# Performance work log

Hardware: AMD Instinct MI355X
Metric: run time of the kernel (lower is better)

Reference implementation:

```python
import jax, jax.numpy as jnp
import numpy as np

N_NODES = 100000


def gcn_conv(x, W, b, src, dst, n_nodes):
    """PyG-style GCNConv: add self-loops, symmetric normalization, aggregate to dst."""
    x = x @ W  # [N, out]
    loop = jnp.arange(n_nodes, dtype=src.dtype)
    src_sl = jnp.concatenate([src, loop])  # [E+N]
    dst_sl = jnp.concatenate([dst, loop])
    deg = jax.ops.segment_sum(jnp.ones(src_sl.shape[0], x.dtype), dst_sl,
                              num_segments=n_nodes)  # [N]
    dinv = jnp.where(deg > 0, jax.lax.rsqrt(deg), 0.0)
    norm = dinv[src_sl] * dinv[dst_sl]  # [E+N]
    msg = x[src_sl] * norm[:, None]  # gather + scale
    out = jax.ops.segment_sum(msg, dst_sl, num_segments=n_nodes)  # scatter-add
    return out + b


def setup_inputs() -> dict:
    key = jax.random.key(0)
    ks = jax.random.split(key, 8)
    in_d, hid_d, out_d = 64, 128, 64
    x = jax.random.normal(ks[0], (N_NODES, in_d), dtype=jnp.float32)
    edge_index = jax.random.randint(ks[1], (2, 1000000), 0, N_NODES, dtype=jnp.int64)
    s1 = 1.0 / np.sqrt(in_d)
    s2 = 1.0 / np.sqrt(hid_d)
    sc = 1.0 / np.sqrt(2 * out_d)
    W1 = jax.random.uniform(ks[2], (in_d, hid_d), jnp.float32, -s1, s1)
    b1 = jnp.zeros((hid_d,), jnp.float32)
    W2 = jax.random.uniform(ks[3], (hid_d, out_d), jnp.float32, -s2, s2)
    b2 = jnp.zeros((out_d,), jnp.float32)
    Wc = jax.random.uniform(ks[4], (2 * out_d, 1), jnp.float32, -sc, sc)
    bc = jax.random.uniform(ks[5], (1,), jnp.float32, -sc, sc)
    return {"x": x, "edge_index": edge_index, "W1": W1, "b1": b1,
            "W2": W2, "b2": b2, "Wc": Wc, "bc": bc}


def reference(x, edge_index, W1, b1, W2, b2, Wc, bc):
    src, dst = edge_index[0], edge_index[1]
    h = jax.nn.relu(gcn_conv(x, W1, b1, src, dst, N_NODES))
    h = jax.nn.relu(gcn_conv(h, W2, b2, src, dst, N_NODES))
    # edge-level gather-concat-linear-sigmoid
    edge_emb = jnp.concatenate([h[src], h[dst]], axis=1)  # [E, 2*out_d]
    logits = edge_emb @ Wc + bc  # [E, 1]
    return jax.nn.sigmoid(logits)
```

## Files before the change

### kernel.cpp

```cpp
#include <hip/hip_runtime.h>
#include <hip/hip_fp16.h>
#include <math.h>

#define IN_D 64
#define HID_D 128
#define OUT_D 64

typedef _Float16 half8 __attribute__((ext_vector_type(8)));
typedef float f32x4 __attribute__((ext_vector_type(4)));

#define ECAP   16384
#define CSRCAP (ECAP + 512 * 3)
#define DCHUNK 2048

__global__ void k_init(int* __restrict__ bcur,
                       const float* __restrict__ W1, const float* __restrict__ W2,
                       __half* __restrict__ w1f, __half* __restrict__ w2f,
                       __half* __restrict__ xs, __half* __restrict__ ts,
                       int N, int nbuk) {
    int t = blockIdx.x * 256 + threadIdx.x;
    if (blockIdx.x == 0 && threadIdx.x < nbuk)
        bcur[threadIdx.x] = threadIdx.x * ECAP;
    if (t < 2048) {
        int which = t >> 10, fl = t & 1023;
        int f = fl >> 6, l = fl & 63, q = l >> 4, n16 = l & 15;
        if (which == 0) {
            int nt = f >> 1, kc = f & 1, n = nt * 16 + n16, k0 = kc * 32 + q * 8;
            for (int j = 0; j < 8; ++j)
                w1f[(size_t)fl * 8 + j] = __float2half(W1[(k0 + j) * 128 + n]);
        } else {
            int nt = f >> 2, kc = f & 3, n = nt * 16 + n16, k0 = kc * 32 + q * 8;
            for (int j = 0; j < 8; ++j)
                w2f[(size_t)fl * 8 + j] = __float2half(W2[(k0 + j) * 64 + n]);
        }
    } else {
        int si = t - 2048;
        if (si < 64) {
            xs[(size_t)N * 64 + si] = __float2half(0.f);
            ts[(size_t)N * 64 + si] = __float2half(0.f);
        }
    }
}

__global__ __launch_bounds__(256) void k_decode3(const unsigned int* __restrict__ raw,
                                                 int E,
                                                 int* __restrict__ bcur,
                                                 int2* __restrict__ pairs) {
    __shared__ int hist[256];
    __shared__ int base[256];
    __shared__ int cnt[256];
    __shared__ int is64s;
    if (threadIdx.x == 0) {
        int f = 1;
        for (int i = 1; i < 64; i += 2) f &= (raw[i] == 0u);
        is64s = f;
    }
    hist[threadIdx.x] = 0; cnt[threadIdx.x] = 0;
    __syncthreads();
    int is64 = is64s;
    int e0 = blockIdx.x * DCHUNK;
    int s[8], d[8], b[8];
    if ((E & 1) == 0) {
#pragma unroll
        for (int i = 0; i < 4; ++i) {
            int e = e0 + (threadIdx.x + i * 256) * 2;
            if (e < E) {
                int s0, d0, s1, d1;
                if (is64) {
                    uint4 sv = *(const uint4*)&raw[2 * (size_t)e];
                    uint4 dv = *(const uint4*)&raw[2 * ((size_t)E + e)];
                    s0 = (int)sv.x; s1 = (int)sv.z;
                    d0 = (int)dv.x; d1 = (int)dv.z;
                } else {
                    uint2 sv = *(const uint2*)&raw[e];
                    uint2 dv = *(const uint2*)&raw[E + e];
                    s0 = (int)sv.x; s1 = (int)sv.y;
                    d0 = (int)dv.x; d1 = (int)dv.y;
                }
                s[2 * i] = s0; d[2 * i] = d0; b[2 * i] = d0 >> 9;
                s[2 * i + 1] = s1; d[2 * i + 1] = d1; b[2 * i + 1] = d1 >> 9;
                atomicAdd(&hist[b[2 * i]], 1);
                atomicAdd(&hist[b[2 * i + 1]], 1);
            } else { b[2 * i] = -1; b[2 * i + 1] = -1; }
        }
    } else {
#pragma unroll
        for (int i = 0; i < 8; ++i) {
            int e = e0 + threadIdx.x + i * 256;
            if (e < E) {
                int sv, dv;
                if (is64) {
                    sv = (int)raw[2 * (size_t)e];
                    dv = (int)raw[2 * ((size_t)E + e)];
                } else {
                    sv = (int)raw[e];
                    dv = (int)raw[E + e];
                }
                s[i] = sv; d[i] = dv; b[i] = dv >> 9;
                atomicAdd(&hist[b[i]], 1);
            } else b[i] = -1;
        }
    }
    __syncthreads();
    if (hist[threadIdx.x] > 0)
        base[threadIdx.x] = atomicAdd(&bcur[threadIdx.x], hist[threadIdx.x]);
    __syncthreads();
#pragma unroll
    for (int i = 0; i < 8; ++i) {
        if (b[i] >= 0) {
            int pos = base[b[i]] + atomicAdd(&cnt[b[i]], 1);
            pairs[pos] = make_int2(s[i], d[i]);
        }
    }
}

__global__ __launch_bounds__(256) void k_build(const int2* __restrict__ pairs,
                                               const int* __restrict__ bcur,
                                               int2* __restrict__ prowdeg,
                                               int* __restrict__ csr_src,
                                               float* __restrict__ dinv,
                                               const float* __restrict__ x,
                                               __half* __restrict__ xs,
                                               int N) {
    __shared__ int deg5[512];
    __shared__ int cur5[512];
    __shared__ int wsum[4];
    int b = blockIdx.x;
    int n0 = b << 9;
    int n1 = n0 + 512; if (n1 > N) n1 = N;
    int nn = n1 - n0;
    deg5[threadIdx.x] = 0;
    deg5[threadIdx.x + 256] = 0;
    __syncthreads();
    int beg = b * ECAP, end = bcur[b];
    for (int i = beg + threadIdx.x; i < end; i += 256)
        atomicAdd(&deg5[pairs[i].y - n0], 1);
    __syncthreads();
    int pbase = b * CSRCAP;
    int t = threadIdx.x;
    int v0 = deg5[2 * t], v1 = deg5[2 * t + 1];
    int p0 = (v0 + 3) & ~3, p1 = (v1 + 3) & ~3;
    int s = p0 + p1;
    int lane = t & 63, w = t >> 6;
    int inc = s;
    for (int off = 1; off < 64; off <<= 1) {
        int n = __shfl_up(inc, off);
        if (lane >= off) inc += n;
    }
    if (lane == 63) wsum[w] = inc;
    __syncthreads();
    for (int k = 0; k < w; ++k) inc += wsum[k];
    int ex0 = inc - s, ex1 = inc - p1;
    int ps0 = pbase + ex0, ps1 = pbase + ex1;
    cur5[2 * t] = ps0;
    cur5[2 * t + 1] = ps1;
    if (2 * t < nn) {
        prowdeg[n0 + 2 * t] = make_int2(ps0, p0);
        dinv[n0 + 2 * t] = rsqrtf((float)v0 + 1.0f);
    }
    if (2 * t + 1 < nn) {
        prowdeg[n0 + 2 * t + 1] = make_int2(ps1, p1);
        dinv[n0 + 2 * t + 1] = rsqrtf((float)v1 + 1.0f);
    }
    __syncthreads();
    for (int i = beg + threadIdx.x; i < end; i += 256) {
        int2 r = pairs[i];
        int pos = atomicAdd(&cur5[r.y - n0], 1);
        csr_src[pos] = r.x;
    }
    __syncthreads();
    for (int i = cur5[2 * t]; i < ps0 + p0; ++i) csr_src[i] = N;
    for (int i = cur5[2 * t + 1]; i < ps1 + p1; ++i) csr_src[i] = N;
    for (int idx = t; idx < nn * 8; idx += 256) {
        int i = idx >> 3, c8 = (idx & 7) * 8;
        int node = n0 + i;
        float di = rsqrtf((float)deg5[i] + 1.0f);
        float4 va = *(const float4*)&x[(size_t)node * 64 + c8];
        float4 vb = *(const float4*)&x[(size_t)node * 64 + c8 + 4];
        union { __half2 h[4]; uint4 u; } pk2;
        pk2.h[0] = __floats2half2_rn(va.x * di, va.y * di);
        pk2.h[1] = __floats2half2_rn(va.z * di, va.w * di);
        pk2.h[2] = __floats2half2_rn(vb.x * di, vb.y * di);
        pk2.h[3] = __floats2half2_rn(vb.z * di, vb.w * di);
        *(uint4*)&xs[(size_t)node * 64 + c8] = pk2.u;
    }
}

__global__ __launch_bounds__(256) void k_gather1(const __half* __restrict__ xs,
                          const float* __restrict__ dinv,
                          const int2* __restrict__ prowdeg, const int* __restrict__ csr,
                          __half* __restrict__ agg, int N) {
    int wv = threadIdx.x >> 6, l = threadIdx.x & 63;
    int ns = l >> 3, seg = l & 7;
    int node = (blockIdx.x * 4 + wv) * 8 + ns;
    bool valid = node < N;
    int nc = valid ? node : N - 1;
    int2 rp = prowdeg[nc];
    int beg = rp.x;
    int pend = beg + (valid ? rp.y : 0);
    float di = dinv[nc];
    half8 hs = *(const half8*)&xs[(size_t)nc * 64 + seg * 8];
    float acc[8];
#pragma unroll
    for (int j = 0; j < 8; ++j) acc[j] = 0.f;
    for (int k = beg; k < pend; k += 4) {
        int4 s4 = *(const int4*)&csr[k];
        half8 h0 = *(const half8*)&xs[(size_t)s4.x * 64 + seg * 8];
        half8 h1 = *(const half8*)&xs[(size_t)s4.y * 64 + seg * 8];
        half8 h2 = *(const half8*)&xs[(size_t)s4.z * 64 + seg * 8];
        half8 h3 = *(const half8*)&xs[(size_t)s4.w * 64 + seg * 8];
#pragma unroll
        for (int j = 0; j < 8; ++j) {
            float t01 = (float)h0[j] + (float)h1[j];
            float t23 = (float)h2[j] + (float)h3[j];
            acc[j] += t01 + t23;
        }
    }
    if (valid) {
        half8 o;
#pragma unroll
        for (int j = 0; j < 8; ++j) o[j] = (_Float16)((acc[j] + (float)hs[j]) * di);
        *(half8*)&agg[(size_t)node * 64 + seg * 8] = o;
    }
}

__global__ __launch_bounds__(256) void k_gather2(const __half* __restrict__ ts,
                          const float* __restrict__ dinv,
                          const int2* __restrict__ prowdeg, const int* __restrict__ csr,
                          const float* __restrict__ b2, const float* __restrict__ Wc,
                          float* __restrict__ s0o, float* __restrict__ s1o, int N) {
    int wv = threadIdx.x >> 6, l = threadIdx.x & 63;
    int ns = l >> 3, seg = l & 7;
    int node = (blockIdx.x * 4 + wv) * 8 + ns;
    bool valid = node < N;
    int nc = valid ? node : N - 1;
    int2 rp = prowdeg[nc];
    int beg = rp.x;
    int pend = beg + (valid ? rp.y : 0);
    float di = dinv[nc];
    half8 hs = *(const half8*)&ts[(size_t)nc * 64 + seg * 8];
    float acc[8];
#pragma unroll
    for (int j = 0; j < 8; ++j) acc[j] = 0.f;
    for (int k = beg; k < pend; k += 4) {
        int4 s4 = *(const int4*)&csr[k];
        half8 h0 = *(const half8*)&ts[(size_t)s4.x * 64 + seg * 8];
        half8 h1 = *(const half8*)&ts[(size_t)s4.y * 64 + seg * 8];
        half8 h2 = *(const half8*)&ts[(size_t)s4.z * 64 + seg * 8];
        half8 h3 = *(const half8*)&ts[(size_t)s4.w * 64 + seg * 8];
#pragma unroll
        for (int j = 0; j < 8; ++j) {
            float t01 = (float)h0[j] + (float)h1[j];
            float t23 = (float)h2[j] + (float)h3[j];
            acc[j] += t01 + t23;
        }
    }
    {
        float4 b2a = *(const float4*)&b2[seg * 8];
        float4 b2b = *(const float4*)&b2[seg * 8 + 4];
        float4 w0a = *(const float4*)&Wc[seg * 8];
        float4 w0b = *(const float4*)&Wc[seg * 8 + 4];
        float4 w1a = *(const float4*)&Wc[64 + seg * 8];
        float4 w1b = *(const float4*)&Wc[64 + seg * 8 + 4];
        float bb[8] = {b2a.x, b2a.y, b2a.z, b2a.w, b2b.x, b2b.y, b2b.z, b2b.w};
        float w0[8] = {w0a.x, w0a.y, w0a.z, w0a.w, w0b.x, w0b.y, w0b.z, w0b.w};
        float w1[8] = {w1a.x, w1a.y, w1a.z, w1a.w, w1b.x, w1b.y, w1b.z, w1b.w};
        float p0 = 0.f, p1 = 0.f;
#pragma unroll
        for (int j = 0; j < 8; ++j) {
            float v = fmaxf((acc[j] + (float)hs[j]) * di + bb[j], 0.f);
            p0 = fmaf(v, w0[j], p0);
            p1 = fmaf(v, w1[j], p1);
        }
        p0 += __shfl_xor(p0, 1); p1 += __shfl_xor(p1, 1);
        p0 += __shfl_xor(p0, 2); p1 += __shfl_xor(p1, 2);
        p0 += __shfl_xor(p0, 4); p1 += __shfl_xor(p1, 4);
        if (seg == 0 && valid) { s0o[node] = p0; s1o[node] = p1; }
    }
}

__global__ __launch_bounds__(256) void k_mlp_mfma(const __half* __restrict__ agg_h,
                                                  const __half* __restrict__ w1f,
                                                  const __half* __restrict__ w2f,
                                                  const float* __restrict__ b1,
                                                  const float* __restrict__ dinv,
                                                  __half* __restrict__ ts, int N) {
    __shared__ __align__(16) __half w1l[8192];
    __shared__ __align__(16) __half w2l[8192];
    {
        const float4* sA = (const float4*)w1f;
        const float4* sB = (const float4*)w2f;
        float4* dA = (float4*)w1l;
        float4* dB = (float4*)w2l;
        for (int i = threadIdx.x; i < 1024; i += 256) { dA[i] = sA[i]; dB[i] = sB[i]; }
    }
    __syncthreads();

    int wv = threadIdx.x >> 6, l = threadIdx.x & 63;
    int m0 = blockIdx.x * 64 + wv * 16;
    if (m0 >= N) return;
    int q = l >> 4, ml = l & 15;
    int rowA = m0 + ml; if (rowA >= N) rowA = N - 1;

    half8 bfr0 = *(const half8*)&agg_h[(size_t)rowA * 64 + q * 8];
    half8 bfr1 = *(const half8*)&agg_h[(size_t)rowA * 64 + 32 + q * 8];

    int pk[8][2];
#pragma unroll
    for (int nt = 0; nt < 8; ++nt) {
        float4 bb = *(const float4*)&b1[nt * 16 + q * 4];
        f32x4 cacc; cacc[0] = bb.x; cacc[1] = bb.y; cacc[2] = bb.z; cacc[3] = bb.w;
        half8 a0 = *(const half8*)&w1l[(nt * 2 + 0) * 512 + l * 8];
        cacc = __builtin_amdgcn_mfma_f32_16x16x32_f16(a0, bfr0, cacc, 0, 0, 0);
        half8 a1 = *(const half8*)&w1l[(nt * 2 + 1) * 512 + l * 8];
        cacc = __builtin_amdgcn_mfma_f32_16x16x32_f16(a1, bfr1, cacc, 0, 0, 0);
        union { __half2 h; int i; } u0, u1;
        u0.h = __floats2half2_rn(fmaxf(cacc[0], 0.f), fmaxf(cacc[1], 0.f));
        u1.h = __floats2half2_rn(fmaxf(cacc[2], 0.f), fmaxf(cacc[3], 0.f));
        pk[nt][0] = u0.i;
        pk[nt][1] = u1.i;
    }

    int src0 = ml + 16 * ((2 * q) & 3);
    int src1 = ml + 16 * ((2 * q + 1) & 3);
    bool hi = (q >= 2);
    half8 afr[4];
#pragma unroll
    for (int kc = 0; kc < 4; ++kc) {
        int t0 = 2 * kc, t1 = 2 * kc + 1;
        int d0a = __shfl(pk[t0][0], src0), d0b = __shfl(pk[t1][0], src0);
        int d1a = __shfl(pk[t0][1], src0), d1b = __shfl(pk[t1][1], src0);
        int d2a = __shfl(pk[t0][0], src1), d2b = __shfl(pk[t1][0], src1);
        int d3a = __shfl(pk[t0][1], src1), d3b = __shfl(pk[t1][1], src1);
        union { int d[4]; half8 h; } u;
        u.d[0] = hi ? d0b : d0a;
        u.d[1] = hi ? d1b : d1a;
        u.d[2] = hi ? d2b : d2a;
        u.d[3] = hi ? d3b : d3a;
        afr[kc] = u.h;
    }

    float dl = dinv[rowA];
    float dv[4];
#pragma unroll
    for (int r = 0; r < 4; ++r) dv[r] = __shfl(dl, q * 4 + r);

#pragma unroll
    for (int nt2 = 0; nt2 < 4; ++nt2) {
        f32x4 cacc; cacc[0] = 0.f; cacc[1] = 0.f; cacc[2] = 0.f; cacc[3] = 0.f;
#pragma unroll
        for (int kc = 0; kc < 4; ++kc) {
            half8 b = *(const half8*)&w2l[(nt2 * 4 + kc) * 512 + l * 8];
            cacc = __builtin_amdgcn_mfma_f32_16x16x32_f16(afr[kc], b, cacc, 0, 0, 0);
        }
#pragma unroll
        for (int r = 0; r < 4; ++r) {
            int node = m0 + q * 4 + r;
            if (node < N)
                ts[(size_t)node * 64 + nt2 * 16 + ml] = __float2half(cacc[r] * dv[r]);
        }
    }
}

__global__ void k_edge(const unsigned int* __restrict__ raw,
                       const float* __restrict__ s0, const float* __restrict__ s1,
                       const float* __restrict__ bc, float* __restrict__ out, int E) {
    __shared__ int is64s;
    if (threadIdx.x == 0) {
        int f = 1;
        for (int i = 1; i < 64; i += 2) f &= (raw[i] == 0u);
        is64s = f;
    }
    __syncthreads();
    int is64 = is64s;
    int e = (blockIdx.x * blockDim.x + threadIdx.x) * 2;
    if (e >= E) return;
    float b = bc[0];
    if (((E & 1) == 0) && (e + 1 < E)) {
        int sa, sb, da, db;
        if (is64) {
            uint4 sv = *(const uint4*)&raw[2 * (size_t)e];
            uint4 dv = *(const uint4*)&raw[2 * ((size_t)E + e)];
            sa = (int)sv.x; sb = (int)sv.z;
            da = (int)dv.x; db = (int)dv.z;
        } else {
            uint2 sv = *(const uint2*)&raw[e];
            uint2 dv = *(const uint2*)&raw[E + e];
            sa = (int)sv.x; sb = (int)sv.y;
            da = (int)dv.x; db = (int)dv.y;
        }
        float z0 = s0[sa] + s1[da] + b;
        float z1 = s0[sb] + s1[db] + b;
        float2 o;
        o.x = 1.0f / (1.0f + __expf(-z0));
        o.y = 1.0f / (1.0f + __expf(-z1));
        *(float2*)&out[e] = o;
    } else {
        for (int k = e; k < E && k < e + 2; ++k) {
            int sa, da;
            if (is64) {
                sa = (int)raw[2 * (size_t)k];
                da = (int)raw[2 * ((size_t)E + k)];
            } else {
                sa = (int)raw[k];
                da = (int)raw[E + k];
            }
            float z = s0[sa] + s1[da] + b;
            out[k] = 1.0f / (1.0f + __expf(-z));
        }
    }
}

extern "C" void kernel_launch(void* const* d_in, const int* in_sizes, int n_in,
                              void* d_out, int out_size, void* d_ws, size_t ws_size,
                              hipStream_t stream) {
    const float* x  = (const float*)d_in[0];
    const unsigned int* eidx = (const unsigned int*)d_in[1];
    const float* W1 = (const float*)d_in[2];
    const float* b1 = (const float*)d_in[3];
    const float* W2 = (const float*)d_in[4];
    const float* b2 = (const float*)d_in[5];
    const float* Wc = (const float*)d_in[6];
    const float* bc = (const float*)d_in[7];
    float* out = (float*)d_out;

    int N = in_sizes[0] / IN_D;
    int E = in_sizes[1] / 2;
    int nbuk = (N + 511) >> 9;
    int nchunk = (E + DCHUNK - 1) / DCHUNK;

    char* p = (char*)d_ws;
    int*   bcur    = (int*)p;    p += 256 * 4;
    int*   csr_src = (int*)p;    p += (size_t)nbuk * CSRCAP * 4;
    float* dinv    = (float*)p;  p += (size_t)N * 4;
    float* s0      = (float*)p;  p += (size_t)N * 4;
    float* s1      = (float*)p;  p += (size_t)N * 4;
    p += 15; p = (char*)((size_t)p & ~(size_t)15);
    int2*  prowdeg = (int2*)p;   p += (size_t)N * 8;
    int2*  pairs   = (int2*)p;   p += (size_t)nbuk * ECAP * 8;
    __half* xs    = (__half*)p;  p += (size_t)(N + 1) * 64 * 2;
    __half* aggh  = (__half*)p;  p += (size_t)N * 64 * 2;
    __half* ts    = (__half*)p;  p += (size_t)(N + 1) * 64 * 2;
    __half* w1f   = (__half*)p;  p += 8192 * 2;
    __half* w2f   = (__half*)p;  p += 8192 * 2;

    k_init<<<9, 256, 0, stream>>>(bcur, W1, W2, w1f, w2f, xs, ts, N, nbuk);
    k_decode3<<<nchunk, 256, 0, stream>>>(eidx, E, bcur, pairs);
    k_build<<<nbuk, 256, 0, stream>>>(pairs, bcur, prowdeg, csr_src, dinv, x, xs, N);

    k_gather1<<<(N + 31) / 32, 256, 0, stream>>>(xs, dinv, prowdeg, csr_src, aggh, N);

    k_mlp_mfma<<<(N + 63) / 64, 256, 0, stream>>>(aggh, w1f, w2f, b1, dinv, ts, N);

    k_gather2<<<(N + 31) / 32, 256, 0, stream>>>(ts, dinv, prowdeg, csr_src,
                                                 b2, Wc, s0, s1, N);

    k_edge<<<(E / 2 + 255) / 256, 256, 0, stream>>>(eidx, s0, s1, bc, out, E);
}
```

Baseline: 193.0 us.

## Halve bucket size, pack edge pairs into one int, split neighbor lists across two lanes

Dst buckets shrink from 512 to 256 nodes, and (src,dst) pairs are packed into a single int (src shifted left, local dst in the low bits), which halves pair traffic between decode and build. CSR rows are padded to multiples of 8, and both gather kernels now give each node two 8-lane slots that walk interleaved edges, then combine them with a shuffle. This doubles gather parallelism per node and halves the pair buffer. The costs are more padding entries and scattered 4-byte index loads in place of int4 loads. Packing src<<8 assumes node ids fit in 23 bits.

```diff
diff --git a/kernel.cpp b/kernel.cpp
--- a/kernel.cpp
+++ b/kernel.cpp
@@ -9,8 +9,10 @@
 typedef _Float16 half8 __attribute__((ext_vector_type(8)));
 typedef float f32x4 __attribute__((ext_vector_type(4)));
 
-#define ECAP   16384
-#define CSRCAP (ECAP + 512 * 3)
+#define NBITS  8
+#define BNODES 256
+#define ECAP   4096
+#define CSRCAP (ECAP + BNODES * 7)
 #define DCHUNK 2048
 
 __global__ void k_init(int* __restrict__ bcur,
@@ -19,8 +21,9 @@
                        __half* __restrict__ xs, __half* __restrict__ ts,
                        int N, int nbuk) {
     int t = blockIdx.x * 256 + threadIdx.x;
-    if (blockIdx.x == 0 && threadIdx.x < nbuk)
-        bcur[threadIdx.x] = threadIdx.x * ECAP;
+    if (blockIdx.x == 0) {
+        for (int i = threadIdx.x; i < nbuk; i += 256) bcur[i] = i * ECAP;
+    }
     if (t < 2048) {
         int which = t >> 10, fl = t & 1023;
         int f = fl >> 6, l = fl & 63, q = l >> 4, n16 = l & 15;
@@ -43,19 +46,19 @@
 }
 
 __global__ __launch_bounds__(256) void k_decode3(const unsigned int* __restrict__ raw,
-                                                 int E,
+                                                 int E, int nbuk,
                                                  int* __restrict__ bcur,
-                                                 int2* __restrict__ pairs) {
-    __shared__ int hist[256];
-    __shared__ int base[256];
-    __shared__ int cnt[256];
+                                                 int* __restrict__ pairs) {
+    __shared__ int hist[512];
+    __shared__ int base[512];
+    __shared__ int cnt[512];
     __shared__ int is64s;
     if (threadIdx.x == 0) {
         int f = 1;
         for (int i = 1; i < 64; i += 2) f &= (raw[i] == 0u);
         is64s = f;
     }
-    hist[threadIdx.x] = 0; cnt[threadIdx.x] = 0;
+    for (int i = threadIdx.x; i < nbuk; i += 256) { hist[i] = 0; cnt[i] = 0; }
     __syncthreads();
     int is64 = is64s;
     int e0 = blockIdx.x * DCHUNK;
@@ -77,8 +80,8 @@
                     s0 = (int)sv.x; s1 = (int)sv.y;
                     d0 = (int)dv.x; d1 = (int)dv.y;
                 }
-                s[2 * i] = s0; d[2 * i] = d0; b[2 * i] = d0 >> 9;
-                s[2 * i + 1] = s1; d[2 * i + 1] = d1; b[2 * i + 1] = d1 >> 9;
+                s[2 * i] = s0; d[2 * i] = d0; b[2 * i] = d0 >> NBITS;
+                s[2 * i + 1] = s1; d[2 * i + 1] = d1; b[2 * i + 1] = d1 >> NBITS;
                 atomicAdd(&hist[b[2 * i]], 1);
                 atomicAdd(&hist[b[2 * i + 1]], 1);
             } else { b[2 * i] = -1; b[2 * i + 1] = -1; }
@@ -96,25 +99,25 @@
                     sv = (int)raw[e];
                     dv = (int)raw[E + e];
                 }
-                s[i] = sv; d[i] = dv; b[i] = dv >> 9;
+                s[i] = sv; d[i] = dv; b[i] = dv >> NBITS;
                 atomicAdd(&hist[b[i]], 1);
             } else b[i] = -1;
         }
     }
     __syncthreads();
-    if (hist[threadIdx.x] > 0)
-        base[threadIdx.x] = atomicAdd(&bcur[threadIdx.x], hist[threadIdx.x]);
+    for (int i = threadIdx.x; i < nbuk; i += 256)
+        if (hist[i] > 0) base[i] = atomicAdd(&bcur[i], hist[i]);
     __syncthreads();
 #pragma unroll
     for (int i = 0; i < 8; ++i) {
         if (b[i] >= 0) {
             int pos = base[b[i]] + atomicAdd(&cnt[b[i]], 1);
-            pairs[pos] = make_int2(s[i], d[i]);
-        }
-    }
-}
-
-__global__ __launch_bounds__(256) void k_build(const int2* __restrict__ pairs,
+            pairs[pos] = (s[i] << NBITS) | (d[i] & (BNODES - 1));
+        }
+    }
+}
+
+__global__ __launch_bounds__(256) void k_build(const int* __restrict__ pairs,
                                                const int* __restrict__ bcur,
                                                int2* __restrict__ prowdeg,
                                                int* __restrict__ csr_src,
@@ -122,27 +125,25 @@
                                                const float* __restrict__ x,
                                                __half* __restrict__ xs,
                                                int N) {
-    __shared__ int deg5[512];
-    __shared__ int cur5[512];
+    __shared__ int deg5[256];
+    __shared__ int cur5[256];
     __shared__ int wsum[4];
     int b = blockIdx.x;
-    int n0 = b << 9;
-    int n1 = n0 + 512; if (n1 > N) n1 = N;
+    int n0 = b << NBITS;
+    int n1 = n0 + BNODES; if (n1 > N) n1 = N;
     int nn = n1 - n0;
     deg5[threadIdx.x] = 0;
-    deg5[threadIdx.x + 256] = 0;
     __syncthreads();
     int beg = b * ECAP, end = bcur[b];
     for (int i = beg + threadIdx.x; i < end; i += 256)
-        atomicAdd(&deg5[pairs[i].y - n0], 1);
+        atomicAdd(&deg5[pairs[i] & (BNODES - 1)], 1);
     __syncthreads();
     int pbase = b * CSRCAP;
     int t = threadIdx.x;
-    int v0 = deg5[2 * t], v1 = deg5[2 * t + 1];
-    int p0 = (v0 + 3) & ~3, p1 = (v1 + 3) & ~3;
-    int s = p0 + p1;
+    int v0 = deg5[t];
+    int p0 = (v0 + 7) & ~7;
     int lane = t & 63, w = t >> 6;
-    int inc = s;
+    int inc = p0;
     for (int off = 1; off < 64; off <<= 1) {
         int n = __shfl_up(inc, off);
         if (lane >= off) inc += n;
@@ -150,27 +151,21 @@
     if (lane == 63) wsum[w] = inc;
     __syncthreads();
     for (int k = 0; k < w; ++k) inc += wsum[k];
-    int ex0 = inc - s, ex1 = inc - p1;
-    int ps0 = pbase + ex0, ps1 = pbase + ex1;
-    cur5[2 * t] = ps0;
-    cur5[2 * t + 1] = ps1;
-    if (2 * t < nn) {
-        prowdeg[n0 + 2 * t] = make_int2(ps0, p0);
-        dinv[n0 + 2 * t] = rsqrtf((float)v0 + 1.0f);
-    }
-    if (2 * t + 1 < nn) {
-        prowdeg[n0 + 2 * t + 1] = make_int2(ps1, p1);
-        dinv[n0 + 2 * t + 1] = rsqrtf((float)v1 + 1.0f);
+    int ex0 = inc - p0;
+    int ps0 = pbase + ex0;
+    cur5[t] = ps0;
+    if (t < nn) {
+        prowdeg[n0 + t] = make_int2(ps0, p0);
+        dinv[n0 + t] = rsqrtf((float)v0 + 1.0f);
     }
     __syncthreads();
     for (int i = beg + threadIdx.x; i < end; i += 256) {
-        int2 r = pairs[i];
-        int pos = atomicAdd(&cur5[r.y - n0], 1);
-        csr_src[pos] = r.x;
-    }
-    __syncthreads();
-    for (int i = cur5[2 * t]; i < ps0 + p0; ++i) csr_src[i] = N;
-    for (int i = cur5[2 * t + 1]; i < ps1 + p1; ++i) csr_src[i] = N;
+        int r = pairs[i];
+        int pos = atomicAdd(&cur5[r & (BNODES - 1)], 1);
+        csr_src[pos] = r >> NBITS;
+    }
+    __syncthreads();
+    for (int i = cur5[t]; i < ps0 + p0; ++i) csr_src[i] = N;
     for (int idx = t; idx < nn * 8; idx += 256) {
         int i = idx >> 3, c8 = (idx & 7) * 8;
         int node = n0 + i;
@@ -191,8 +186,8 @@
                           const int2* __restrict__ prowdeg, const int* __restrict__ csr,
                           __half* __restrict__ agg, int N) {
     int wv = threadIdx.x >> 6, l = threadIdx.x & 63;
-    int ns = l >> 3, seg = l & 7;
-    int node = (blockIdx.x * 4 + wv) * 8 + ns;
+    int ns = l >> 4, slot = (l >> 3) & 1, seg = l & 7;
+    int node = (blockIdx.x * 4 + wv) * 4 + ns;
     bool valid = node < N;
     int nc = valid ? node : N - 1;
     int2 rp = prowdeg[nc];
@@ -203,12 +198,12 @@
     float acc[8];
 #pragma unroll
     for (int j = 0; j < 8; ++j) acc[j] = 0.f;
-    for (int k = beg; k < pend; k += 4) {
-        int4 s4 = *(const int4*)&csr[k];
-        half8 h0 = *(const half8*)&xs[(size_t)s4.x * 64 + seg * 8];
-        half8 h1 = *(const half8*)&xs[(size_t)s4.y * 64 + seg * 8];
-        half8 h2 = *(const half8*)&xs[(size_t)s4.z * 64 + seg * 8];
-        half8 h3 = *(const half8*)&xs[(size_t)s4.w * 64 + seg * 8];
+    for (int k = beg + slot; k < pend; k += 8) {
+        int s0 = csr[k], s1 = csr[k + 2], s2 = csr[k + 4], s3 = csr[k + 6];
+        half8 h0 = *(const half8*)&xs[(size_t)s0 * 64 + seg * 8];
+        half8 h1 = *(const half8*)&xs[(size_t)s1 * 64 + seg * 8];
+        half8 h2 = *(const half8*)&xs[(size_t)s2 * 64 + seg * 8];
+        half8 h3 = *(const half8*)&xs[(size_t)s3 * 64 + seg * 8];
 #pragma unroll
         for (int j = 0; j < 8; ++j) {
             float t01 = (float)h0[j] + (float)h1[j];
@@ -216,7 +211,9 @@
             acc[j] += t01 + t23;
         }
     }
-    if (valid) {
+#pragma unroll
+    for (int j = 0; j < 8; ++j) acc[j] += __shfl_xor(acc[j], 8);
+    if (slot == 0 && valid) {
         half8 o;
 #pragma unroll
         for (int j = 0; j < 8; ++j) o[j] = (_Float16)((acc[j] + (float)hs[j]) * di);
@@ -230,8 +227,8 @@
                           const float* __restrict__ b2, const float* __restrict__ Wc,
                           float* __restrict__ s0o, float* __restrict__ s1o, int N) {
     int wv = threadIdx.x >> 6, l = threadIdx.x & 63;
-    int ns = l >> 3, seg = l & 7;
-    int node = (blockIdx.x * 4 + wv) * 8 + ns;
+    int ns = l >> 4, slot = (l >> 3) & 1, seg = l & 7;
+    int node = (blockIdx.x * 4 + wv) * 4 + ns;
     bool valid = node < N;
     int nc = valid ? node : N - 1;
     int2 rp = prowdeg[nc];
@@ -242,12 +239,12 @@
     float acc[8];
 #pragma unroll
     for (int j = 0; j < 8; ++j) acc[j] = 0.f;
-    for (int k = beg; k < pend; k += 4) {
-        int4 s4 = *(const int4*)&csr[k];
-        half8 h0 = *(const half8*)&ts[(size_t)s4.x * 64 + seg * 8];
-        half8 h1 = *(const half8*)&ts[(size_t)s4.y * 64 + seg * 8];
-        half8 h2 = *(const half8*)&ts[(size_t)s4.z * 64 + seg * 8];
-        half8 h3 = *(const half8*)&ts[(size_t)s4.w * 64 + seg * 8];
+    for (int k = beg + slot; k < pend; k += 8) {
+        int s0 = csr[k], s1 = csr[k + 2], s2 = csr[k + 4], s3 = csr[k + 6];
+        half8 h0 = *(const half8*)&ts[(size_t)s0 * 64 + seg * 8];
+        half8 h1 = *(const half8*)&ts[(size_t)s1 * 64 + seg * 8];
+        half8 h2 = *(const half8*)&ts[(size_t)s2 * 64 + seg * 8];
+        half8 h3 = *(const half8*)&ts[(size_t)s3 * 64 + seg * 8];
 #pragma unroll
         for (int j = 0; j < 8; ++j) {
             float t01 = (float)h0[j] + (float)h1[j];
@@ -255,7 +252,9 @@
             acc[j] += t01 + t23;
         }
     }
-    {
+#pragma unroll
+    for (int j = 0; j < 8; ++j) acc[j] += __shfl_xor(acc[j], 8);
+    if (slot == 0) {
         float4 b2a = *(const float4*)&b2[seg * 8];
         float4 b2b = *(const float4*)&b2[seg * 8 + 4];
         float4 w0a = *(const float4*)&Wc[seg * 8];
@@ -426,18 +425,18 @@
 
     int N = in_sizes[0] / IN_D;
     int E = in_sizes[1] / 2;
-    int nbuk = (N + 511) >> 9;
+    int nbuk = (N + BNODES - 1) >> NBITS;
     int nchunk = (E + DCHUNK - 1) / DCHUNK;
 
     char* p = (char*)d_ws;
-    int*   bcur    = (int*)p;    p += 256 * 4;
+    int*   bcur    = (int*)p;    p += 512 * 4;
     int*   csr_src = (int*)p;    p += (size_t)nbuk * CSRCAP * 4;
     float* dinv    = (float*)p;  p += (size_t)N * 4;
     float* s0      = (float*)p;  p += (size_t)N * 4;
     float* s1      = (float*)p;  p += (size_t)N * 4;
     p += 15; p = (char*)((size_t)p & ~(size_t)15);
     int2*  prowdeg = (int2*)p;   p += (size_t)N * 8;
-    int2*  pairs   = (int2*)p;   p += (size_t)nbuk * ECAP * 8;
+    int*   pairs   = (int*)p;    p += (size_t)nbuk * ECAP * 4;
     __half* xs    = (__half*)p;  p += (size_t)(N + 1) * 64 * 2;
     __half* aggh  = (__half*)p;  p += (size_t)N * 64 * 2;
     __half* ts    = (__half*)p;  p += (size_t)(N + 1) * 64 * 2;
@@ -445,14 +444,14 @@
     __half* w2f   = (__half*)p;  p += 8192 * 2;
 
     k_init<<<9, 256, 0, stream>>>(bcur, W1, W2, w1f, w2f, xs, ts, N, nbuk);
-    k_decode3<<<nchunk, 256, 0, stream>>>(eidx, E, bcur, pairs);
+    k_decode3<<<nchunk, 256, 0, stream>>>(eidx, E, nbuk, bcur, pairs);
     k_build<<<nbuk, 256, 0, stream>>>(pairs, bcur, prowdeg, csr_src, dinv, x, xs, N);
 
-    k_gather1<<<(N + 31) / 32, 256, 0, stream>>>(xs, dinv, prowdeg, csr_src, aggh, N);
+    k_gather1<<<(N + 15) / 16, 256, 0, stream>>>(xs, dinv, prowdeg, csr_src, aggh, N);
 
     k_mlp_mfma<<<(N + 63) / 64, 256, 0, stream>>>(aggh, w1f, w2f, b1, dinv, ts, N);
 
-    k_gather2<<<(N + 31) / 32, 256, 0, stream>>>(ts, dinv, prowdeg, csr_src,
+    k_gather2<<<(N + 15) / 16, 256, 0, stream>>>(ts, dinv, prowdeg, csr_src,
                                                  b2, Wc, s0, s1, N);
 
     k_edge<<<(E / 2 + 255) / 256, 256, 0, stream>>>(eidx, s0, s1, bc, out, E);
```

Result: faster. 182.1 us (-5.7%).
